# Optimization experiments

Measured on AMD Instinct MI355X. Metric: run time of the kernel, lower is better.

## Reference

```python
import jax, jax.numpy as jnp
import numpy as np

G = 512          # graphs in batch
NPG = 128        # nodes per graph (equal-sized so decoder batches)
TEMP = 0.1       # SimilarityDecoder temperature


def setup_inputs() -> dict:
    key = jax.random.key(0)
    ks = jax.random.split(key, 10)
    N, D, K, H, T = G * NPG, 512, 1024, 128, 10
    return {
        "x": jax.random.normal(ks[0], (N, D), jnp.float32),
        "batch": jnp.repeat(jnp.arange(G, dtype=jnp.int64), NPG),
        "codebook_input": jax.random.normal(ks[1], (K, D), jnp.float32),
        "fc1_w": jax.random.normal(ks[2], (H, D), jnp.float32) * (1.0 / np.sqrt(D)),
        "fc1_b": jax.random.normal(ks[3], (H,), jnp.float32) * 0.01,
        "fc2_w": jax.random.normal(ks[4], (D, H), jnp.float32) * (1.0 / np.sqrt(H)),
        "fc2_b": jax.random.normal(ks[5], (D,), jnp.float32) * 0.01,
        "causal": jax.random.normal(ks[6], (K, K), jnp.float32),
        "cls_w": jax.random.normal(ks[7], (T, D), jnp.float32) * (1.0 / np.sqrt(D)),
        "cls_b": jax.random.normal(ks[8], (T,), jnp.float32) * 0.01,
    }


def _segment_mean(v, batch, num_segments):
    s = jax.ops.segment_sum(v, batch, num_segments=num_segments)
    cnt = jax.ops.segment_sum(jnp.ones((v.shape[0], 1), v.dtype), batch, num_segments=num_segments)
    return s / jnp.maximum(cnt, 1.0)


def _batched_adj(z):
    # SimilarityDecoder: per-graph sigmoid(norm_z @ norm_z.T / temp); graphs equal-sized -> [G, n, n]
    zg = z.reshape(G, NPG, -1)
    zn = zg / jnp.maximum(jnp.linalg.norm(zg, axis=-1, keepdims=True), 1e-12)
    return jax.nn.sigmoid(jnp.einsum("gnd,gmd->gnm", zn, zn) / TEMP)


def reference(x, batch, codebook_input, fc1_w, fc1_b, fc2_w, fc2_b, causal, cls_w, cls_b):
    K = causal.shape[0]
    I = jnp.eye(K, dtype=x.dtype)

    # ---- VectorQuantizer ----
    h = jax.nn.sigmoid(codebook_input @ fc1_w.T + fc1_b)
    codebook_transformed = h @ fc2_w.T + fc2_b                 # [K, D]
    causal_effect = causal * (1.0 - I) + I                     # off-diag causal + identity
    cs = jax.nn.sigmoid(codebook_transformed)
    causal_diag = causal * I
    causal_cb = causal_effect @ (causal_diag @ cs)             # [K, D]
    counter_matrix = causal * (1.0 - I)                        # DegreeLayer assumed: off-diagonal mask
    counter_cb = causal_effect @ (counter_matrix @ cs)         # [K, D]

    # ---- ClassLayer ----
    pooled_x = _segment_mean(x, batch, G)                      # [G, D]
    # squared euclidean distances x vs causal_cb -> argmin codebook index
    d2 = (jnp.sum(x * x, 1, keepdims=True)
          - 2.0 * (x @ causal_cb.T)
          + jnp.sum(causal_cb * causal_cb, 1))                 # [N, K]
    idx = jnp.argmin(d2, axis=1)                               # [N]
    causal_nodes = x + causal_cb[idx]
    counter_nodes = counter_cb[idx]
    z_nodes = codebook_transformed[idx]                        # [N, D]
    pooled_causal = _segment_mean(causal_nodes, batch, G)
    pooled_counter = _segment_mean(counter_nodes, batch, G)
    causal_pre = pooled_causal @ cls_w.T + cls_b
    counter_pre = pooled_counter @ cls_w.T + cls_b
    y_pre = pooled_x @ jax.lax.stop_gradient(cls_w).T + jax.lax.stop_gradient(cls_b)

    # ---- SimilarityDecoder ----
    A_ori = _batched_adj(x)                                    # [G, n, n]
    A_rec = _batched_adj(z_nodes)

    return (causal_pre, counter_pre, y_pre, A_ori, A_rec,
            z_nodes, x, causal_diag, counter_matrix, pooled_causal, pooled_x)
```

## Files before the change

kernel.cpp:

```cpp
#include <hip/hip_runtime.h>
#include <math.h>

#define NG   512
#define NPG  128
#define NN   65536
#define DD   512
#define KK   1024
#define HH   128
#define TT   10

#define RES_TAU 1.0f
#define RES_CAP 65536

typedef __attribute__((ext_vector_type(8))) short short8;
typedef __attribute__((ext_vector_type(4))) float float4v;
typedef __attribute__((ext_vector_type(4))) float        f32x4;
typedef __attribute__((ext_vector_type(4))) unsigned int u32x4;
typedef __attribute__((ext_vector_type(4))) unsigned short u16x4;

static const long OFF_CPRE = 0;
static const long OFF_KPRE = 5120;
static const long OFF_YPRE = 10240;
static const long OFF_AORI = 15360;
static const long OFF_AREC = OFF_AORI + 8388608L;
static const long OFF_Z    = OFF_AREC + 8388608L;
static const long OFF_X    = OFF_Z + 33554432L;
static const long OFF_CD   = OFF_X + 33554432L;
static const long OFF_CM   = OFF_CD + 1048576L;
static const long OFF_PC   = OFF_CM + 1048576L;
static const long OFF_PX   = OFF_PC + 262144L;

__device__ __forceinline__ float sigm_fast(float v) { return 1.0f / (1.0f + __expf(-v)); }
__device__ __forceinline__ float sigm_acc (float v) { return 1.0f / (1.0f + expf(-v)); }

__global__ void k_diagmask(const float* __restrict__ causal,
                           float* __restrict__ cd, float* __restrict__ cm,
                           float* __restrict__ dv) {
  int i = blockIdx.x * 256 + threadIdx.x;
  int r = i >> 10, c = i & 1023;
  float v = causal[i];
  bool diag = (r == c);
  cd[i] = diag ? v : 0.0f;
  cm[i] = diag ? 0.0f : v;
  if (diag) dv[r] = v;
}

__global__ void k_fc1(const float* __restrict__ cbi, const float* __restrict__ w,
                      const float* __restrict__ b, float* __restrict__ h) {
  int i = blockIdx.x * 256 + threadIdx.x;
  int k = i >> 7, j = i & 127;
  const float4* xr = (const float4*)(cbi + (long)k * DD);
  const float4* wr = (const float4*)(w + (long)j * DD);
  float s = b[j];
  for (int d = 0; d < DD / 4; d++) {
    float4 a = xr[d], bb = wr[d];
    s += a.x * bb.x + a.y * bb.y + a.z * bb.z + a.w * bb.w;
  }
  h[i] = sigm_acc(s);
}

__global__ void k_fc2(const float* __restrict__ h, const float* __restrict__ w,
                      const float* __restrict__ b, float* __restrict__ ct,
                      float* __restrict__ cs) {
  int i = blockIdx.x * 256 + threadIdx.x;
  int k = i >> 9, d = i & 511;
  const float4* hr = (const float4*)(h + (long)k * HH);
  const float4* wr = (const float4*)(w + (long)d * HH);
  float s = b[d];
  for (int j = 0; j < HH / 4; j++) {
    float4 a = hr[j], bb = wr[j];
    s += a.x * bb.x + a.y * bb.y + a.z * bb.z + a.w * bb.w;
  }
  ct[i] = s;
  cs[i] = sigm_acc(s);
}

template <int AM, int BM>
__launch_bounds__(256)
__global__ void gemm64(const float* __restrict__ A, const float* __restrict__ B,
                       const float* __restrict__ dscale, float* __restrict__ C,
                       int M, int Nc, int Kr) {
  __shared__ __align__(16) float as[32][68];
  __shared__ __align__(16) float bs[32][68];
  int tid = threadIdx.x;
  int tx = tid & 15, ty = tid >> 4;
  int m0 = blockIdx.y * 64, n0 = blockIdx.x * 64;
  float acc[4][4] = {};
  for (int kt = 0; kt < Kr; kt += 32) {
    for (int s = tid; s < 512; s += 256) {
      int m = s >> 3, c4 = (s & 7) << 2;
      int gr = m0 + m, gc = kt + c4;
      float4 v = *(const float4*)&A[(long)gr * Kr + gc];
      float vv[4] = {v.x, v.y, v.z, v.w};
      if (AM == 1) {
#pragma unroll
        for (int q = 0; q < 4; q++) if (gc + q == gr) vv[q] = 1.0f;
      } else if (AM == 2) {
#pragma unroll
        for (int q = 0; q < 4; q++) if (gc + q == gr) vv[q] = 0.0f;
      }
      as[c4 + 0][m] = vv[0]; as[c4 + 1][m] = vv[1];
      as[c4 + 2][m] = vv[2]; as[c4 + 3][m] = vv[3];
    }
    for (int s = tid; s < 512; s += 256) {
      int r = s >> 4, c4 = (s & 15) << 2;
      float4 v = *(const float4*)&B[(long)(kt + r) * Nc + n0 + c4];
      if (BM == 1) {
        float sc = dscale[kt + r];
        v.x *= sc; v.y *= sc; v.z *= sc; v.w *= sc;
      }
      *(float4*)&bs[r][c4] = v;
    }
    __syncthreads();
#pragma unroll
    for (int r = 0; r < 32; r++) {
      float4 a4 = *(const float4*)&as[r][ty * 4];
      float4 b4 = *(const float4*)&bs[r][tx * 4];
      float av[4] = {a4.x, a4.y, a4.z, a4.w};
      float bv[4] = {b4.x, b4.y, b4.z, b4.w};
#pragma unroll
      for (int i = 0; i < 4; i++)
#pragma unroll
        for (int j = 0; j < 4; j++) acc[i][j] += av[i] * bv[j];
    }
    __syncthreads();
  }
#pragma unroll
  for (int i = 0; i < 4; i++) {
    float4 v = make_float4(acc[i][0], acc[i][1], acc[i][2], acc[i][3]);
    *(float4*)&C[(long)(m0 + ty * 4 + i) * Nc + n0 + tx * 4] = v;
  }
}

__launch_bounds__(256)
__global__ void gemm64_dual(const float* __restrict__ A, const float* __restrict__ B,
                            const float* __restrict__ dscale,
                            float* __restrict__ Cz, float* __restrict__ Ci,
                            int M, int Nc, int Kr) {
  __shared__ __align__(16) float asZ[32][68];
  __shared__ __align__(16) float asI[32][68];
  __shared__ __align__(16) float bs[32][68];
  __shared__ float dsc[32];
  int tid = threadIdx.x;
  int tx = tid & 15, ty = tid >> 4;
  int m0 = blockIdx.y * 64, n0 = blockIdx.x * 64;
  float accZ[4][4] = {};
  float accI[4][4] = {};
  for (int kt = 0; kt < Kr; kt += 32) {
    for (int s = tid; s < 512; s += 256) {
      int m = s >> 3, c4 = (s & 7) << 2;
      int gr = m0 + m, gc = kt + c4;
      float4 v = *(const float4*)&A[(long)gr * Kr + gc];
      float vz[4] = {v.x, v.y, v.z, v.w};
      float vi[4] = {v.x, v.y, v.z, v.w};
#pragma unroll
      for (int q = 0; q < 4; q++) if (gc + q == gr) { vz[q] = 0.0f; vi[q] = 1.0f; }
      asZ[c4 + 0][m] = vz[0]; asZ[c4 + 1][m] = vz[1];
      asZ[c4 + 2][m] = vz[2]; asZ[c4 + 3][m] = vz[3];
      asI[c4 + 0][m] = vi[0]; asI[c4 + 1][m] = vi[1];
      asI[c4 + 2][m] = vi[2]; asI[c4 + 3][m] = vi[3];
    }
    for (int s = tid; s < 512; s += 256) {
      int r = s >> 4, c4 = (s & 15) << 2;
      float4 v = *(const float4*)&B[(long)(kt + r) * Nc + n0 + c4];
      *(float4*)&bs[r][c4] = v;
    }
    if (tid < 32) dsc[tid] = dscale[kt + tid];
    __syncthreads();
#pragma unroll
    for (int r = 0; r < 32; r++) {
      float4 aZ = *(const float4*)&asZ[r][ty * 4];
      float4 aI = *(const float4*)&asI[r][ty * 4];
      float4 b4 = *(const float4*)&bs[r][tx * 4];
      float sc = dsc[r];
      float az[4] = {aZ.x, aZ.y, aZ.z, aZ.w};
      float ai[4] = {aI.x, aI.y, aI.z, aI.w};
      float bz[4] = {b4.x, b4.y, b4.z, b4.w};
      float bi[4] = {b4.x * sc, b4.y * sc, b4.z * sc, b4.w * sc};
#pragma unroll
      for (int i = 0; i < 4; i++)
#pragma unroll
        for (int j = 0; j < 4; j++) {
          accZ[i][j] += az[i] * bz[j];
          accI[i][j] += ai[i] * bi[j];
        }
    }
    __syncthreads();
  }
#pragma unroll
  for (int i = 0; i < 4; i++) {
    float4 vz = make_float4(accZ[i][0], accZ[i][1], accZ[i][2], accZ[i][3]);
    float4 vi = make_float4(accI[i][0], accI[i][1], accI[i][2], accI[i][3]);
    *(float4*)&Cz[(long)(m0 + ty * 4 + i) * Nc + n0 + tx * 4] = vz;
    *(float4*)&Ci[(long)(m0 + ty * 4 + i) * Nc + n0 + tx * 4] = vi;
  }
}

__global__ void k_cnorm(const float* __restrict__ ccb, float* __restrict__ cn2,
                        int* __restrict__ rc) {
  if (blockIdx.x == 0 && threadIdx.x == 0) *rc = 0;
  int row = blockIdx.x * 4 + (threadIdx.x >> 6);
  int lane = threadIdx.x & 63;
  const float* r = ccb + (long)row * DD;
  float s = 0.0f;
  for (int q = 0; q < DD; q += 64) { float v = r[lane + q]; s += v * v; }
  for (int off = 32; off > 0; off >>= 1) s += __shfl_down(s, off);
  if (lane == 0) cn2[row] = s;
}

__device__ __forceinline__ ushort bf16_rne(float f, float* back) {
  unsigned int b = __float_as_uint(f);
  unsigned int r = b + 0x7fffu + ((b >> 16) & 1u);
  ushort h = (ushort)(r >> 16);
  *back = __uint_as_float(((unsigned int)h) << 16);
  return h;
}

__global__ void k_split(const float4* __restrict__ src, ushort* __restrict__ hi,
                        ushort* __restrict__ lo, long n4) {
  long i = (long)blockIdx.x * 256 + threadIdx.x;
  if (i >= n4) return;
  float4 v = src[i];
  float vv[4] = {v.x, v.y, v.z, v.w};
  ushort h[4], l[4];
#pragma unroll
  for (int q = 0; q < 4; q++) {
    float back;
    h[q] = bf16_rne(vv[q], &back);
    float rem = vv[q] - back;
    float dummy;
    l[q] = bf16_rne(rem, &dummy);
  }
  ((ushort4*)hi)[i] = make_ushort4(h[0], h[1], h[2], h[3]);
  ((ushort4*)lo)[i] = make_ushort4(l[0], l[1], l[2], l[3]);
}

__global__ void k_split_nt(const float* __restrict__ src, ushort* __restrict__ hi,
                           ushort* __restrict__ lo, long n4) {
  long i = (long)blockIdx.x * 256 + threadIdx.x;
  if (i >= n4) return;
  f32x4 v = __builtin_nontemporal_load((const f32x4*)src + i);
  ushort h[4], l[4];
#pragma unroll
  for (int q = 0; q < 4; q++) {
    float back;
    h[q] = bf16_rne(v[q], &back);
    float rem = v[q] - back;
    float dummy;
    l[q] = bf16_rne(rem, &dummy);
  }
  u16x4 hv = {h[0], h[1], h[2], h[3]};
  u16x4 lv = {l[0], l[1], l[2], l[3]};
  __builtin_nontemporal_store(hv, (u16x4*)hi + i);
  __builtin_nontemporal_store(lv, (u16x4*)lo + i);
}

__launch_bounds__(512, 2)
__global__ void k_argmin_mfma(const ushort* __restrict__ xh, const ushort* __restrict__ xl,
                              const ushort* __restrict__ ch, const ushort* __restrict__ cl,
                              const float* __restrict__ cn2, int* __restrict__ idxg,
                              int* __restrict__ rc, int* __restrict__ rlist) {
  __shared__ __align__(16) ushort xsh[64 * 512];
  __shared__ __align__(16) ushort xsl[64 * 512];
  __shared__ float cn2s[KK];
  __shared__ float mm1[8][64], mm2[8][64];
  __shared__ int   mid[8][64];

  int tid = threadIdx.x;
  long n0 = (long)blockIdx.x * 64;

  u32x4 tmp[16];
#pragma unroll
  for (int r = 0; r < 16; r++) {
    int g = tid + r * 512;
    int rid = g >> 6;
    int node = rid & 63;
    int gb = (g & 63) << 4;
    const ushort* src = ((rid < 64) ? xh : xl) + (n0 + node) * (long)DD;
    tmp[r] = __builtin_nontemporal_load((const u32x4*)((const char*)src + gb));
  }
  for (int s = tid; s < KK; s += 512) cn2s[s] = cn2[s];
#pragma unroll
  for (int r = 0; r < 16; r++) {
    int g = tid + r * 512;
    int rid = g >> 6;
    int node = rid & 63;
    int gb = (g & 63) << 4;
    int db = gb ^ ((node & 7) << 4);
    ushort* dst = (rid < 64) ? xsh : xsl;
    *(u32x4*)((char*)dst + node * 1024 + db) = tmp[r];
  }
  __syncthreads();

  int lane = tid & 63, wave = tid >> 6;
  int col = lane & 15, quad = lane >> 4;

  int abase[4];
#pragma unroll
  for (int i = 0; i < 4; i++) {
    int node = i * 16 + col;
    abase[i] = node * 1024 + ((quad ^ (node & 3)) << 4) + (((node >> 2) & 1) << 6);
  }

  const ushort* pBh[4];
  const ushort* pBl[4];
#pragma unroll
  for (int j = 0; j < 4; j++) {
    long row = (long)(wave * 64 + j * 16 + col);
    pBh[j] = ch + row * DD + quad * 8;
    pBl[j] = cl + row * DD + quad * 8;
  }

  float m1[16], m2[16]; int id1[16];
#pragma unroll
  for (int s = 0; s < 16; s++) { m1[s] = 3.4e38f; m2[s] = 3.4e38f; id1[s] = 0; }

  const float4v vzero = {0.0f, 0.0f, 0.0f, 0.0f};
  float4v acc[4][4];
  short8 aH[4], aL[4];
  short8 bh0[4], bl0[4], bh1[4], bl1[4];

#define LDA(K)                                                                   \
  do {                                                                           \
    int k_ = (K);                                                                \
    _Pragma("unroll") for (int i = 0; i < 4; i++) {                              \
      int ao_ = abase[i] ^ (k_ << 6);                                            \
      aH[i] = *(const short8*)((const char*)xsh + ao_);                          \
      aL[i] = *(const short8*)((const char*)xsl + ao_);                          \
    }                                                                            \
  } while (0)

#define LDB(K, BH, BL)                                                           \
  do {                                                                           \
    int k_ = (K);                                                                \
    _Pragma("unroll") for (int j = 0; j < 4; j++) {                              \
      BH[j] = *(const short8*)(pBh[j] + k_ * 32);                                \
      BL[j] = *(const short8*)(pBl[j] + k_ * 32);                                \
    }                                                                            \
  } while (0)

#define COMP(BH, BL)                                                             \
  do {                                                                           \
    __builtin_amdgcn_s_setprio(1);                                               \
    _Pragma("unroll") for (int j = 0; j < 4; j++)                                \
      _Pragma("unroll") for (int i = 0; i < 4; i++) {                            \
        acc[i][j] = __builtin_amdgcn_mfma_f32_16x16x32_bf16(aH[i], BH[j], acc[i][j], 0, 0, 0); \
        acc[i][j] = __builtin_amdgcn_mfma_f32_16x16x32_bf16(aH[i], BL[j], acc[i][j], 0, 0, 0); \
        acc[i][j] = __builtin_amdgcn_mfma_f32_16x16x32_bf16(aL[i], BH[j], acc[i][j], 0, 0, 0); \
      }                                                                          \
    __builtin_amdgcn_s_setprio(0);                                               \
  } while (0)

  for (int cc = 0; cc < 2; cc++) {
#pragma unroll
    for (int i = 0; i < 4; i++)
#pragma unroll
      for (int j = 0; j < 4; j++) acc[i][j] = vzero;

    LDB(0, bh0, bl0);
#pragma unroll 1
    for (int k = 0; k < 16; k += 2) {
      LDA(k);
      LDB(k + 1, bh1, bl1);
      __builtin_amdgcn_sched_barrier(0);
      COMP(bh0, bl0);
      __builtin_amdgcn_sched_barrier(0);
      LDA(k + 1);
      LDB((k + 2) & 15, bh0, bl0);
      __builtin_amdgcn_sched_barrier(0);
      COMP(bh1, bl1);
      __builtin_amdgcn_sched_barrier(0);
    }

    int cb0 = cc * 512 + wave * 64;
#pragma unroll
    for (int j = 0; j < 4; j++) {
      int code = cb0 + j * 16 + col;
      float c2 = cn2s[code];
#pragma unroll
      for (int i = 0; i < 4; i++) {
#pragma unroll
        for (int r = 0; r < 4; r++) {
          float v = fmaf(-2.0f, acc[i][j][r], c2);
          int s = i * 4 + r;
          if (v < m1[s] || (v == m1[s] && code < id1[s])) {
            m2[s] = m1[s]; m1[s] = v; id1[s] = code;
          } else if (v < m2[s]) {
            m2[s] = v;
          }
        }
      }
    }
#pragma unroll
    for (int j = 0; j < 4; j++) { pBh[j] += 512 * DD; pBl[j] += 512 * DD; }
  }
#undef LDA
#undef LDB
#undef COMP

#pragma unroll
  for (int s = 0; s < 16; s++) {
#pragma unroll
    for (int mask = 1; mask <= 8; mask <<= 1) {
      float om1 = __shfl_xor(m1[s], mask);
      float om2 = __shfl_xor(m2[s], mask);
      int   oid = __shfl_xor(id1[s], mask);
      if (om1 < m1[s] || (om1 == m1[s] && oid < id1[s])) {
        m2[s] = fminf(m1[s], om2); m1[s] = om1; id1[s] = oid;
      } else {
        m2[s] = fminf(m2[s], om1);
      }
    }
  }
  if (col == 0) {
#pragma unroll
    for (int s = 0; s < 16; s++) {
      int i = s >> 2, r = s & 3;
      int nl = i * 16 + quad * 4 + r;
      mm1[wave][nl] = m1[s]; mm2[wave][nl] = m2[s]; mid[wave][nl] = id1[s];
    }
  }
  __syncthreads();
  if (tid < 64) {
    float f1 = mm1[0][tid], f2 = mm2[0][tid]; int fi = mid[0][tid];
#pragma unroll
    for (int w = 1; w < 8; w++) {
      float b1 = mm1[w][tid], b2 = mm2[w][tid]; int bi = mid[w][tid];
      if (b1 < f1 || (b1 == f1 && bi < fi)) {
        f2 = fminf(f1, b2); f1 = b1; fi = bi;
      } else {
        f2 = fminf(f2, b1);
      }
    }
    idxg[n0 + tid] = fi;
    if (f2 - f1 < RES_TAU) {
      int p = atomicAdd(rc, 1);
      if (p < RES_CAP) rlist[p] = (int)(n0 + tid);
    }
  }
}

__global__ void k_rescue(const float* __restrict__ x, const float* __restrict__ ccb,
                         const float* __restrict__ cn2, const int* __restrict__ rc,
                         const int* __restrict__ rlist, int* __restrict__ idxg) {
  __shared__ float xs[DD];
  __shared__ float bv[256]; __shared__ int bi[256];
  int count = *rc; if (count > RES_CAP) count = RES_CAP;
  int tid = threadIdx.x;
  for (int f = blockIdx.x; f < count; f += gridDim.x) {
    int n = rlist[f];
    for (int s = tid; s < DD; s += 256) xs[s] = x[(long)n * DD + s];
    __syncthreads();
    float best = 3.4e38f; int besti = 0;
    for (int c = tid; c < KK; c += 256) {
      const float4* cr = (const float4*)(ccb + (long)c * DD);
      const float4* xr = (const float4*)xs;
      float dot = 0.0f;
      for (int d = 0; d < DD / 4; d++) {
        float4 a = xr[d], b = cr[d];
        dot += a.x * b.x + a.y * b.y + a.z * b.z + a.w * b.w;
      }
      float v = cn2[c] - 2.0f * dot;
      if (v < best || (v == best && c < besti)) { best = v; besti = c; }
    }
    bv[tid] = best; bi[tid] = besti;
    __syncthreads();
    for (int off = 128; off > 0; off >>= 1) {
      if (tid < off) {
        float ov = bv[tid + off]; int oi = bi[tid + off];
        if (ov < bv[tid] || (ov == bv[tid] && oi < bi[tid])) { bv[tid] = ov; bi[tid] = oi; }
      }
      __syncthreads();
    }
    if (tid == 0) idxg[n] = bi[0];
    __syncthreads();
  }
}

__global__ void k_gather(const float4* __restrict__ ct4, const int* __restrict__ idxg,
                         float4* __restrict__ z4) {
  long i = (long)blockIdx.x * 256 + threadIdx.x;
  int n = (int)(i >> 7), c = (int)(i & 127);
  z4[i] = ct4[(long)idxg[n] * 128 + c];
}

__global__ void k_pool(const float* __restrict__ x, const float* __restrict__ ccb,
                       const float* __restrict__ kcb, const int* __restrict__ idxg,
                       float* __restrict__ px, float* __restrict__ pc,
                       float* __restrict__ pk) {
  __shared__ int sidx[NPG];
  int g = blockIdx.x, tid = threadIdx.x;
  if (tid < NPG) sidx[tid] = idxg[g * NPG + tid];
  __syncthreads();
  int d = tid;
  float sx = 0.0f, sc = 0.0f, sk = 0.0f;
  for (int n = 0; n < NPG; n++) {
    sx += x[((long)g * NPG + n) * DD + d];
    long r = (long)sidx[n] * DD + d;
    sc += ccb[r]; sk += kcb[r];
  }
  px[(long)g * DD + d] = sx / 128.0f;
  pc[(long)g * DD + d] = (sx + sc) / 128.0f;
  pk[(long)g * DD + d] = sk / 128.0f;
}

__global__ void k_heads(const float* __restrict__ pc, const float* __restrict__ pk,
                        const float* __restrict__ px, const float* __restrict__ w,
                        const float* __restrict__ b, float* __restrict__ cpre,
                        float* __restrict__ kpre, float* __restrict__ ypre) {
  int g = blockIdx.x, t = threadIdx.x;
  if (t >= 30) return;
  int which = t / 10, tt = t % 10;
  const float* src = (which == 0) ? pc : ((which == 1) ? pk : px);
  const float* sr = src + (long)g * DD;
  const float* wr = w + (long)tt * DD;
  float s = 0.0f;
  for (int d = 0; d < DD; d++) s += sr[d] * wr[d];
  s += b[tt];
  float* dst = (which == 0) ? cpre : ((which == 1) ? kpre : ypre);
  dst[g * TT + tt] = s;
}

__global__ void k_copy(const float* __restrict__ src, float* __restrict__ dst) {
  long i = (long)blockIdx.x * 256 + threadIdx.x;
  f32x4 v = __builtin_nontemporal_load((const f32x4*)src + i);
  __builtin_nontemporal_store(v, (f32x4*)dst + i);
}

__launch_bounds__(256)
__global__ void k_adj(const float* __restrict__ Z, float* __restrict__ Aout) {
  __shared__ float nrm[NPG];
  __shared__ float inv[NPG];
  __shared__ __align__(16) float zs[32][132];
  int tid = threadIdx.x;
  int g = blockIdx.x;
  const float* base = Z + (long)g * NPG * DD;
  if (tid < NPG) nrm[tid] = 0.0f;
  __syncthreads();
  for (int k = 0; k < 64; k++) {
    long i = (long)k * 256 + tid;
    int n = (int)(i >> 7);
    float4 v = ((const float4*)base)[i];
    float s = v.x * v.x + v.y * v.y + v.z * v.z + v.w * v.w;
    for (int off = 32; off > 0; off >>= 1) s += __shfl_down(s, off);
    if ((tid & 63) == 0) atomicAdd(&nrm[n], s);
  }
  __syncthreads();
  if (tid < NPG) inv[tid] = 1.0f / fmaxf(sqrtf(nrm[tid]), 1e-12f);
  __syncthreads();
  float acc[8][8] = {};
  int tx = tid & 15, ty = tid >> 4;
  for (int dt = 0; dt < DD; dt += 32) {
    for (int s = tid; s < 1024; s += 256) {
      int n = s >> 3, c4 = (s & 7) << 2;
      float4 v = *(const float4*)&base[(long)n * DD + dt + c4];
      float iv = inv[n];
      zs[c4 + 0][n] = v.x * iv; zs[c4 + 1][n] = v.y * iv;
      zs[c4 + 2][n] = v.z * iv; zs[c4 + 3][n] = v.w * iv;
    }
    __syncthreads();
#pragma unroll 8
    for (int r = 0; r < 32; r++) {
      float rv[8], cv[8];
      *(float4*)&rv[0] = *(const float4*)&zs[r][ty * 8];
      *(float4*)&rv[4] = *(const float4*)&zs[r][ty * 8 + 4];
      *(float4*)&cv[0] = *(const float4*)&zs[r][tx * 8];
      *(float4*)&cv[4] = *(const float4*)&zs[r][tx * 8 + 4];
#pragma unroll
      for (int i = 0; i < 8; i++)
#pragma unroll
        for (int j = 0; j < 8; j++) acc[i][j] += rv[i] * cv[j];
    }
    __syncthreads();
  }
  float* aout = Aout + (long)g * NPG * NPG;
#pragma unroll
  for (int i = 0; i < 8; i++) {
    int rr = ty * 8 + i;
    float o[8];
#pragma unroll
    for (int j = 0; j < 8; j++) o[j] = sigm_fast(acc[i][j] * 10.0f);
    *(float4*)&aout[(long)rr * NPG + tx * 8]     = make_float4(o[0], o[1], o[2], o[3]);
    *(float4*)&aout[(long)rr * NPG + tx * 8 + 4] = make_float4(o[4], o[5], o[6], o[7]);
  }
}

extern "C" void kernel_launch(void* const* d_in, const int* in_sizes, int n_in,
                              void* d_out, int out_size, void* d_ws, size_t ws_size,
                              hipStream_t stream) {
  const float* x      = (const float*)d_in[0];
  const float* cbi    = (const float*)d_in[2];
  const float* fc1w   = (const float*)d_in[3];
  const float* fc1b   = (const float*)d_in[4];
  const float* fc2w   = (const float*)d_in[5];
  const float* fc2b   = (const float*)d_in[6];
  const float* causal = (const float*)d_in[7];
  const float* clsw   = (const float*)d_in[8];
  const float* clsb   = (const float*)d_in[9];
  float* out = (float*)d_out;

  float* cpre = out + OFF_CPRE;
  float* kpre = out + OFF_KPRE;
  float* ypre = out + OFF_YPRE;

  float* scr  = out + OFF_AORI;
  float* h    = scr;
  float* cs   = scr + 131072L;
  float* tmp2 = scr + 655360L;
  float* ccb  = scr + 1179648L;
  float* kcb  = scr + 1703936L;
  float* cn2  = scr + 2228224L;
  int*   idxg = (int*)(scr + 2229248L);
  float* pk   = scr + 2294784L;
  float* dv   = scr + 2556928L;
  ushort* ch  = (ushort*)(scr + 2557952L);
  ushort* cl  = (ushort*)(scr + 2820096L);
  int*   rc   = (int*)(scr + 3082240L);
  int*   rlist= (int*)(scr + 3082496L);
  float* ct   = out + OFF_AREC;
  ushort* xh  = (ushort*)(out + OFF_X);
  ushort* xl  = (ushort*)(out + OFF_X + 16777216L);

  k_diagmask<<<4096, 256, 0, stream>>>(causal, out + OFF_CD, out + OFF_CM, dv);
  k_fc1<<<512, 256, 0, stream>>>(cbi, fc1w, fc1b, h);
  k_fc2<<<2048, 256, 0, stream>>>(h, fc2w, fc2b, ct, cs);
  gemm64_dual<<<dim3(8, 16), 256, 0, stream>>>(causal, cs, dv, tmp2, ccb, KK, DD, KK);
  gemm64<1, 0><<<dim3(8, 16), 256, 0, stream>>>(causal, tmp2, nullptr, kcb, KK, DD, KK);
  k_cnorm<<<256, 256, 0, stream>>>(ccb, cn2, rc);
  k_split_nt<<<32768, 256, 0, stream>>>(x, xh, xl, 8388608L);
  k_split<<<512, 256, 0, stream>>>((const float4*)ccb, ch, cl, 131072L);
  k_argmin_mfma<<<1024, 512, 0, stream>>>(xh, xl, ch, cl, cn2, idxg, rc, rlist);
  k_rescue<<<128, 256, 0, stream>>>(x, ccb, cn2, rc, rlist, idxg);
  k_gather<<<32768, 256, 0, stream>>>((const float4*)ct, idxg, (float4*)(out + OFF_Z));
  k_pool<<<512, 512, 0, stream>>>(x, ccb, kcb, idxg, out + OFF_PX, out + OFF_PC, pk);
  k_heads<<<512, 64, 0, stream>>>(out + OFF_PC, pk, out + OFF_PX, clsw, clsb, cpre, kpre, ypre);
  k_copy<<<32768, 256, 0, stream>>>(x, out + OFF_X);
  k_adj<<<512, 256, 0, stream>>>(out + OFF_Z, out + OFF_AREC);
  k_adj<<<512, 256, 0, stream>>>(x, out + OFF_AORI);
}
```

Before: 1.680 ms.

## Shrink argmin tile to 16 nodes per block with 4 waves

Restructures the MFMA argmin kernel so each 256-thread block handles 16 nodes instead of 64, and each wave covers 64 codes per pass over 4 code chunks instead of a 4x4 register tile. The explicit double-buffered B loads, sched barriers and the LDS copy of code norms are dropped in favour of a simpler fully unrolled loop that reads norms from global memory. The aim is more blocks and higher occupancy with less LDS and fewer registers. The cost is far less reuse of each codebook fragment, since every B load now feeds one A row tile instead of four, which raises codebook traffic from L2 by about four times.

```diff
diff --git a/kernel.cpp b/kernel.cpp
--- a/kernel.cpp
+++ b/kernel.cpp
@@ -255,39 +255,37 @@
   __builtin_nontemporal_store(lv, (u16x4*)lo + i);
 }
 
-__launch_bounds__(512, 2)
+__launch_bounds__(256, 4)
 __global__ void k_argmin_mfma(const ushort* __restrict__ xh, const ushort* __restrict__ xl,
                               const ushort* __restrict__ ch, const ushort* __restrict__ cl,
                               const float* __restrict__ cn2, int* __restrict__ idxg,
                               int* __restrict__ rc, int* __restrict__ rlist) {
-  __shared__ __align__(16) ushort xsh[64 * 512];
-  __shared__ __align__(16) ushort xsl[64 * 512];
-  __shared__ float cn2s[KK];
-  __shared__ float mm1[8][64], mm2[8][64];
-  __shared__ int   mid[8][64];
+  __shared__ __align__(16) ushort xsh[16 * 512];
+  __shared__ __align__(16) ushort xsl[16 * 512];
+  __shared__ float mm1[4][16], mm2[4][16];
+  __shared__ int   mid[4][16];
 
   int tid = threadIdx.x;
-  long n0 = (long)blockIdx.x * 64;
-
-  u32x4 tmp[16];
-#pragma unroll
-  for (int r = 0; r < 16; r++) {
-    int g = tid + r * 512;
+  long n0 = (long)blockIdx.x * 16;
+
+  u32x4 tmp[8];
+#pragma unroll
+  for (int r = 0; r < 8; r++) {
+    int g = tid + r * 256;
     int rid = g >> 6;
-    int node = rid & 63;
+    int node = rid & 15;
     int gb = (g & 63) << 4;
-    const ushort* src = ((rid < 64) ? xh : xl) + (n0 + node) * (long)DD;
+    const ushort* src = ((rid < 16) ? xh : xl) + (n0 + node) * (long)DD;
     tmp[r] = __builtin_nontemporal_load((const u32x4*)((const char*)src + gb));
   }
-  for (int s = tid; s < KK; s += 512) cn2s[s] = cn2[s];
-#pragma unroll
-  for (int r = 0; r < 16; r++) {
-    int g = tid + r * 512;
+#pragma unroll
+  for (int r = 0; r < 8; r++) {
+    int g = tid + r * 256;
     int rid = g >> 6;
-    int node = rid & 63;
+    int node = rid & 15;
     int gb = (g & 63) << 4;
     int db = gb ^ ((node & 7) << 4);
-    ushort* dst = (rid < 64) ? xsh : xsl;
+    ushort* dst = (rid < 16) ? xsh : xsl;
     *(u32x4*)((char*)dst + node * 1024 + db) = tmp[r];
   }
   __syncthreads();
@@ -295,12 +293,7 @@
   int lane = tid & 63, wave = tid >> 6;
   int col = lane & 15, quad = lane >> 4;
 
-  int abase[4];
-#pragma unroll
-  for (int i = 0; i < 4; i++) {
-    int node = i * 16 + col;
-    abase[i] = node * 1024 + ((quad ^ (node & 3)) << 4) + (((node >> 2) & 1) << 6);
-  }
+  int abase = col * 1024 + ((quad ^ (col & 3)) << 4) + (((col >> 2) & 1) << 6);
 
   const ushort* pBh[4];
   const ushort* pBl[4];
@@ -311,95 +304,60 @@
     pBl[j] = cl + row * DD + quad * 8;
   }
 
-  float m1[16], m2[16]; int id1[16];
-#pragma unroll
-  for (int s = 0; s < 16; s++) { m1[s] = 3.4e38f; m2[s] = 3.4e38f; id1[s] = 0; }
+  float m1[4], m2[4]; int id1[4];
+#pragma unroll
+  for (int s = 0; s < 4; s++) { m1[s] = 3.4e38f; m2[s] = 3.4e38f; id1[s] = 0; }
 
   const float4v vzero = {0.0f, 0.0f, 0.0f, 0.0f};
-  float4v acc[4][4];
-  short8 aH[4], aL[4];
-  short8 bh0[4], bl0[4], bh1[4], bl1[4];
-
-#define LDA(K)                                                                   \
-  do {                                                                           \
-    int k_ = (K);                                                                \
-    _Pragma("unroll") for (int i = 0; i < 4; i++) {                              \
-      int ao_ = abase[i] ^ (k_ << 6);                                            \
-      aH[i] = *(const short8*)((const char*)xsh + ao_);                          \
-      aL[i] = *(const short8*)((const char*)xsl + ao_);                          \
-    }                                                                            \
-  } while (0)
-
-#define LDB(K, BH, BL)                                                           \
-  do {                                                                           \
-    int k_ = (K);                                                                \
-    _Pragma("unroll") for (int j = 0; j < 4; j++) {                              \
-      BH[j] = *(const short8*)(pBh[j] + k_ * 32);                                \
-      BL[j] = *(const short8*)(pBl[j] + k_ * 32);                                \
-    }                                                                            \
-  } while (0)
-
-#define COMP(BH, BL)                                                             \
-  do {                                                                           \
-    __builtin_amdgcn_s_setprio(1);                                               \
-    _Pragma("unroll") for (int j = 0; j < 4; j++)                                \
-      _Pragma("unroll") for (int i = 0; i < 4; i++) {                            \
-        acc[i][j] = __builtin_amdgcn_mfma_f32_16x16x32_bf16(aH[i], BH[j], acc[i][j], 0, 0, 0); \
-        acc[i][j] = __builtin_amdgcn_mfma_f32_16x16x32_bf16(aH[i], BL[j], acc[i][j], 0, 0, 0); \
-        acc[i][j] = __builtin_amdgcn_mfma_f32_16x16x32_bf16(aL[i], BH[j], acc[i][j], 0, 0, 0); \
-      }                                                                          \
-    __builtin_amdgcn_s_setprio(0);                                               \
-  } while (0)
-
-  for (int cc = 0; cc < 2; cc++) {
-#pragma unroll
-    for (int i = 0; i < 4; i++)
-#pragma unroll
-      for (int j = 0; j < 4; j++) acc[i][j] = vzero;
-
-    LDB(0, bh0, bl0);
+  float4v acc[4];
+
 #pragma unroll 1
-    for (int k = 0; k < 16; k += 2) {
-      LDA(k);
-      LDB(k + 1, bh1, bl1);
-      __builtin_amdgcn_sched_barrier(0);
-      COMP(bh0, bl0);
-      __builtin_amdgcn_sched_barrier(0);
-      LDA(k + 1);
-      LDB((k + 2) & 15, bh0, bl0);
-      __builtin_amdgcn_sched_barrier(0);
-      COMP(bh1, bl1);
-      __builtin_amdgcn_sched_barrier(0);
-    }
-
-    int cb0 = cc * 512 + wave * 64;
+  for (int cc = 0; cc < 4; cc++) {
+#pragma unroll
+    for (int j = 0; j < 4; j++) acc[j] = vzero;
+
+#pragma unroll
+    for (int k = 0; k < 16; k++) {
+      int ao = abase ^ (k << 6);
+      short8 aH = *(const short8*)((const char*)xsh + ao);
+      short8 aL = *(const short8*)((const char*)xsl + ao);
+      short8 bh[4], bl[4];
+#pragma unroll
+      for (int j = 0; j < 4; j++) {
+        bh[j] = *(const short8*)(pBh[j] + k * 32);
+        bl[j] = *(const short8*)(pBl[j] + k * 32);
+      }
+      __builtin_amdgcn_s_setprio(1);
+#pragma unroll
+      for (int j = 0; j < 4; j++) {
+        acc[j] = __builtin_amdgcn_mfma_f32_16x16x32_bf16(aH, bh[j], acc[j], 0, 0, 0);
+        acc[j] = __builtin_amdgcn_mfma_f32_16x16x32_bf16(aH, bl[j], acc[j], 0, 0, 0);
+        acc[j] = __builtin_amdgcn_mfma_f32_16x16x32_bf16(aL, bh[j], acc[j], 0, 0, 0);
+      }
+      __builtin_amdgcn_s_setprio(0);
+    }
+
+    int cb0 = cc * 256 + wave * 64;
 #pragma unroll
     for (int j = 0; j < 4; j++) {
       int code = cb0 + j * 16 + col;
-      float c2 = cn2s[code];
-#pragma unroll
-      for (int i = 0; i < 4; i++) {
-#pragma unroll
-        for (int r = 0; r < 4; r++) {
-          float v = fmaf(-2.0f, acc[i][j][r], c2);
-          int s = i * 4 + r;
-          if (v < m1[s] || (v == m1[s] && code < id1[s])) {
-            m2[s] = m1[s]; m1[s] = v; id1[s] = code;
-          } else if (v < m2[s]) {
-            m2[s] = v;
-          }
+      float c2 = cn2[code];
+#pragma unroll
+      for (int r = 0; r < 4; r++) {
+        float v = fmaf(-2.0f, acc[j][r], c2);
+        if (v < m1[r] || (v == m1[r] && code < id1[r])) {
+          m2[r] = m1[r]; m1[r] = v; id1[r] = code;
+        } else if (v < m2[r]) {
+          m2[r] = v;
         }
       }
     }
 #pragma unroll
-    for (int j = 0; j < 4; j++) { pBh[j] += 512 * DD; pBl[j] += 512 * DD; }
-  }
-#undef LDA
-#undef LDB
-#undef COMP
-
-#pragma unroll
-  for (int s = 0; s < 16; s++) {
+    for (int j = 0; j < 4; j++) { pBh[j] += 256 * DD; pBl[j] += 256 * DD; }
+  }
+
+#pragma unroll
+  for (int s = 0; s < 4; s++) {
 #pragma unroll
     for (int mask = 1; mask <= 8; mask <<= 1) {
       float om1 = __shfl_xor(m1[s], mask);
@@ -414,17 +372,16 @@
   }
   if (col == 0) {
 #pragma unroll
-    for (int s = 0; s < 16; s++) {
-      int i = s >> 2, r = s & 3;
-      int nl = i * 16 + quad * 4 + r;
+    for (int s = 0; s < 4; s++) {
+      int nl = quad * 4 + s;
       mm1[wave][nl] = m1[s]; mm2[wave][nl] = m2[s]; mid[wave][nl] = id1[s];
     }
   }
   __syncthreads();
-  if (tid < 64) {
+  if (tid < 16) {
     float f1 = mm1[0][tid], f2 = mm2[0][tid]; int fi = mid[0][tid];
 #pragma unroll
-    for (int w = 1; w < 8; w++) {
+    for (int w = 1; w < 4; w++) {
       float b1 = mm1[w][tid], b2 = mm2[w][tid]; int bi = mid[w][tid];
       if (b1 < f1 || (b1 == f1 && bi < fi)) {
         f2 = fminf(f1, b2); f1 = b1; fi = bi;
@@ -629,7 +586,7 @@
   k_cnorm<<<256, 256, 0, stream>>>(ccb, cn2, rc);
   k_split_nt<<<32768, 256, 0, stream>>>(x, xh, xl, 8388608L);
   k_split<<<512, 256, 0, stream>>>((const float4*)ccb, ch, cl, 131072L);
-  k_argmin_mfma<<<1024, 512, 0, stream>>>(xh, xl, ch, cl, cn2, idxg, rc, rlist);
+  k_argmin_mfma<<<4096, 256, 0, stream>>>(xh, xl, ch, cl, cn2, idxg, rc, rlist);
   k_rescue<<<128, 256, 0, stream>>>(x, ccb, cn2, rc, rlist, idxg);
   k_gather<<<32768, 256, 0, stream>>>((const float4*)ct, idxg, (float4*)(out + OFF_Z));
   k_pool<<<512, 512, 0, stream>>>(x, ccb, kcb, idxg, out + OFF_PX, out + OFF_PC, pk);
```

Result: slower. 2.217 ms (+32.0%).

## Compute per-graph similarity adjacency with split-bf16 MFMA instead of FP32 FMA

Applied to the files above, without the earlier changes.

Rewrites the adjacency kernel to normalize rows, split them into high/low bf16 parts stored in swizzled shared memory, and compute the Gram matrix with three bf16 MFMA products per tile. The block grows to 512 threads and stages half the feature dimension at a time. This targets the FP32 vector-ALU cost of the per-graph 128x128x512 products, at the cost of large shared memory use (limiting occupancy), slight precision loss from dropping the low*low term, and less coalesced scalar output stores.

```diff
diff --git a/kernel.cpp b/kernel.cpp
--- a/kernel.cpp
+++ b/kernel.cpp
@@ -527,18 +527,20 @@
   __builtin_nontemporal_store(v, (f32x4*)dst + i);
 }
 
-__launch_bounds__(256)
+__launch_bounds__(512)
 __global__ void k_adj(const float* __restrict__ Z, float* __restrict__ Aout) {
   __shared__ float nrm[NPG];
   __shared__ float inv[NPG];
-  __shared__ __align__(16) float zs[32][132];
+  __shared__ __align__(16) ushort zh[NPG * 256];
+  __shared__ __align__(16) ushort zl[NPG * 256];
+
   int tid = threadIdx.x;
   int g = blockIdx.x;
   const float* base = Z + (long)g * NPG * DD;
   if (tid < NPG) nrm[tid] = 0.0f;
   __syncthreads();
-  for (int k = 0; k < 64; k++) {
-    long i = (long)k * 256 + tid;
+  for (int k = 0; k < 32; k++) {
+    long i = (long)k * 512 + tid;
     int n = (int)(i >> 7);
     float4 v = ((const float4*)base)[i];
     float s = v.x * v.x + v.y * v.y + v.z * v.z + v.w * v.w;
@@ -547,41 +549,84 @@
   }
   __syncthreads();
   if (tid < NPG) inv[tid] = 1.0f / fmaxf(sqrtf(nrm[tid]), 1e-12f);
-  __syncthreads();
-  float acc[8][8] = {};
-  int tx = tid & 15, ty = tid >> 4;
-  for (int dt = 0; dt < DD; dt += 32) {
-    for (int s = tid; s < 1024; s += 256) {
-      int n = s >> 3, c4 = (s & 7) << 2;
-      float4 v = *(const float4*)&base[(long)n * DD + dt + c4];
-      float iv = inv[n];
-      zs[c4 + 0][n] = v.x * iv; zs[c4 + 1][n] = v.y * iv;
-      zs[c4 + 2][n] = v.z * iv; zs[c4 + 3][n] = v.w * iv;
-    }
-    __syncthreads();
-#pragma unroll 8
-    for (int r = 0; r < 32; r++) {
-      float rv[8], cv[8];
-      *(float4*)&rv[0] = *(const float4*)&zs[r][ty * 8];
-      *(float4*)&rv[4] = *(const float4*)&zs[r][ty * 8 + 4];
-      *(float4*)&cv[0] = *(const float4*)&zs[r][tx * 8];
-      *(float4*)&cv[4] = *(const float4*)&zs[r][tx * 8 + 4];
-#pragma unroll
-      for (int i = 0; i < 8; i++)
-#pragma unroll
-        for (int j = 0; j < 8; j++) acc[i][j] += rv[i] * cv[j];
-    }
-    __syncthreads();
-  }
+
+  int lane = tid & 63, wave = tid >> 6;
+  int col = lane & 15, quad = lane >> 4;
+  int wy = wave >> 1, wx = wave & 1;
+
+  const float4v vzero = {0.0f, 0.0f, 0.0f, 0.0f};
+  float4v acc[2][4];
+#pragma unroll
+  for (int i = 0; i < 2; i++)
+#pragma unroll
+    for (int j = 0; j < 4; j++) acc[i][j] = vzero;
+
+  for (int half = 0; half < 2; half++) {
+    __syncthreads();
+    for (int it = 0; it < 8; it++) {
+      int gi = tid + it * 512;
+      int row = gi >> 5;
+      int gr  = gi & 31;
+      const float4* src = (const float4*)(base + (long)row * DD + half * 256 + gr * 8);
+      float4 v0 = src[0], v1 = src[1];
+      float iv = inv[row];
+      float vv[8] = {v0.x * iv, v0.y * iv, v0.z * iv, v0.w * iv,
+                     v1.x * iv, v1.y * iv, v1.z * iv, v1.w * iv};
+      short8 hv, lv;
+#pragma unroll
+      for (int q = 0; q < 8; q++) {
+        float back, dummy;
+        hv[q] = (short)bf16_rne(vv[q], &back);
+        lv[q] = (short)bf16_rne(vv[q] - back, &dummy);
+      }
+      int db = (gr << 4) ^ ((row & 7) << 4);
+      *(short8*)((char*)zh + row * 512 + db) = hv;
+      *(short8*)((char*)zl + row * 512 + db) = lv;
+    }
+    __syncthreads();
+#pragma unroll
+    for (int k = 0; k < 8; k++) {
+      short8 bh[4], bl[4];
+#pragma unroll
+      for (int j = 0; j < 4; j++) {
+        int ro = wx * 64 + j * 16 + col;
+        int ao = ro * 512 + ((((k << 6) | (quad << 4))) ^ ((ro & 7) << 4));
+        bh[j] = *(const short8*)((const char*)zh + ao);
+        bl[j] = *(const short8*)((const char*)zl + ao);
+      }
+      short8 ah[2], al[2];
+#pragma unroll
+      for (int i = 0; i < 2; i++) {
+        int ro = wy * 32 + i * 16 + col;
+        int ao = ro * 512 + ((((k << 6) | (quad << 4))) ^ ((ro & 7) << 4));
+        ah[i] = *(const short8*)((const char*)zh + ao);
+        al[i] = *(const short8*)((const char*)zl + ao);
+      }
+      __builtin_amdgcn_s_setprio(1);
+#pragma unroll
+      for (int j = 0; j < 4; j++)
+#pragma unroll
+        for (int i = 0; i < 2; i++) {
+          acc[i][j] = __builtin_amdgcn_mfma_f32_16x16x32_bf16(ah[i], bh[j], acc[i][j], 0, 0, 0);
+          acc[i][j] = __builtin_amdgcn_mfma_f32_16x16x32_bf16(ah[i], bl[j], acc[i][j], 0, 0, 0);
+          acc[i][j] = __builtin_amdgcn_mfma_f32_16x16x32_bf16(al[i], bh[j], acc[i][j], 0, 0, 0);
+        }
+      __builtin_amdgcn_s_setprio(0);
+    }
+  }
+
   float* aout = Aout + (long)g * NPG * NPG;
 #pragma unroll
-  for (int i = 0; i < 8; i++) {
-    int rr = ty * 8 + i;
-    float o[8];
-#pragma unroll
-    for (int j = 0; j < 8; j++) o[j] = sigm_fast(acc[i][j] * 10.0f);
-    *(float4*)&aout[(long)rr * NPG + tx * 8]     = make_float4(o[0], o[1], o[2], o[3]);
-    *(float4*)&aout[(long)rr * NPG + tx * 8 + 4] = make_float4(o[4], o[5], o[6], o[7]);
+  for (int i = 0; i < 2; i++) {
+#pragma unroll
+    for (int r = 0; r < 4; r++) {
+      int a = wy * 32 + i * 16 + quad * 4 + r;
+#pragma unroll
+      for (int j = 0; j < 4; j++) {
+        int b = wx * 64 + j * 16 + col;
+        aout[(long)a * NPG + b] = sigm_fast(acc[i][j][r] * 10.0f);
+      }
+    }
   }
 }
 
@@ -635,6 +680,6 @@
   k_pool<<<512, 512, 0, stream>>>(x, ccb, kcb, idxg, out + OFF_PX, out + OFF_PC, pk);
   k_heads<<<512, 64, 0, stream>>>(out + OFF_PC, pk, out + OFF_PX, clsw, clsb, cpre, kpre, ypre);
   k_copy<<<32768, 256, 0, stream>>>(x, out + OFF_X);
-  k_adj<<<512, 256, 0, stream>>>(out + OFF_Z, out + OFF_AREC);
-  k_adj<<<512, 256, 0, stream>>>(x, out + OFF_AORI);
-}
+  k_adj<<<512, 512, 0, stream>>>(out + OFF_Z, out + OFF_AREC);
+  k_adj<<<512, 512, 0, stream>>>(x, out + OFF_AORI);
+}
```

New measurement: 1.531 ms. 8.9% less time.
